# Optimization experiments

Hardware: AMD Instinct MI355X
Metric: run time of the kernel (lower is better)

Reference implementation:

```python
import jax, jax.numpy as jnp
import numpy as np

N_EMBD = 1568  # 2 * 784, hard-coded in the source module
HEAD_SIZE = 128
BATCH = 16384


def setup_inputs() -> dict:
    key = jax.random.key(0)
    kx, kq, kk, kv = jax.random.split(key, 4)
    x = jax.random.normal(kx, (BATCH, N_EMBD), dtype=jnp.float32)
    wq = jax.random.normal(kq, (N_EMBD, HEAD_SIZE), dtype=jnp.float32) * (N_EMBD ** -0.5)
    wk = jax.random.normal(kk, (N_EMBD, HEAD_SIZE), dtype=jnp.float32) * (N_EMBD ** -0.5)
    wv = jax.random.normal(kv, (N_EMBD, HEAD_SIZE), dtype=jnp.float32) * (N_EMBD ** -0.5)
    return {"x": x, "wq": wq, "wk": wk, "wv": wv}


def reference(x, wq, wk, wv):
    # x: [B, N]; projections (bias-free Linear): [B, H]
    B, N = x.shape
    q = x @ wq
    k = x @ wk
    v = x @ wv
    # Outer-product score matrix per batch element: [B, H, H]
    attn = jnp.einsum('bi,bj->bij', q, k) * (N ** -0.5)  # scale uses FEATURE dim N, as in source
    attn = jax.nn.softmax(attn, axis=-1)
    # dropout is identity in eval mode
    out = jnp.einsum('bij,bj->bi', attn, v)  # [B, H]
    return out
```

## Files before the change

kernel.cpp:

```cpp
#include <hip/hip_runtime.h>
#include <stdint.h>

typedef unsigned short u16;
typedef __bf16 bf16x8 __attribute__((ext_vector_type(8)));
typedef float f32x4 __attribute__((ext_vector_type(4)));

#define M_ROWS 16384
#define K_DIM  1568
#define H_DIM  128
#define NQ     384
#define MT     32
#define BK     32
#define NSTEP  49
#define K0LEN  768
#define K1LEN  800
#define ASTR   808
#define PSTR   132
#define KSTRIDE (NQ * BK)
#define SCALE  0.02525381361380526f
#define LOG2E  1.4426950408889634f

__device__ __forceinline__ u16 f32_to_bf16_rne(float f) {
    uint32_t u = __float_as_uint(f);
    uint32_t r = (u + 0x7FFFu + ((u >> 16) & 1u)) >> 16;
    return (u16)r;
}

#define MFMA(a, b, c) __builtin_amdgcn_mfma_f32_16x16x32_bf16(a, b, c, 0, 0, 0)

__global__ __launch_bounds__(256) void wtrans_kernel(
    const float* __restrict__ wq, const float* __restrict__ wk,
    const float* __restrict__ wv, u16* __restrict__ wt2)
{
    __shared__ u16 tile[32][33];
    const float* w = (blockIdx.z == 0) ? wq : (blockIdx.z == 1) ? wk : wv;
    const int k0 = blockIdx.x * 32;
    const int nloc0 = blockIdx.y * 32;
    const int ng0 = blockIdx.z * 128 + nloc0;

    const int tn = threadIdx.x & 31;
    const int tk = threadIdx.x >> 5;
    #pragma unroll
    for (int p = 0; p < 4; p++) {
        int kk = tk + p * 8;
        tile[kk][tn] = f32_to_bf16_rne(w[(size_t)(k0 + kk) * H_DIM + nloc0 + tn]);
    }
    __syncthreads();

    const int klo = threadIdx.x & 31;
    const int tn2 = threadIdx.x >> 5;
    u16* dst = wt2 + (size_t)(k0 >> 5) * KSTRIDE;
    #pragma unroll
    for (int p = 0; p < 4; p++) {
        int nn = tn2 + p * 8;
        dst[(size_t)(ng0 + nn) * 32 + klo] = tile[klo][nn];
    }
}

__global__ __launch_bounds__(512) void fused_kernel(
    const float* __restrict__ x,
    const u16* __restrict__ wt2,
    float* __restrict__ out)
{
    __shared__ char smem[MT * ASTR * 2];
    u16*  Abuf = (u16*)smem;
    float (*Pq)[PSTR] = (float (*)[PSTR])smem;
    float (*Pk)[PSTR] = (float (*)[PSTR])(smem + MT * PSTR * 4);
    float (*Pv)[PSTR] = (float (*)[PSTR])(smem + 2 * MT * PSTR * 4);

    const int tid  = threadIdx.x;
    const int lane = tid & 63;
    const int wave = tid >> 6;
    const int lrow = lane & 15;
    const int quad = lane >> 4;
    const int m0   = blockIdx.x * MT;

    const u16* bp[3];
    #pragma unroll
    for (int nt = 0; nt < 3; nt++) {
        int ng = wave * 48 + nt * 16 + lrow;
        bp[nt] = wt2 + (size_t)ng * 32 + quad * 8;
    }

    const int srow = tid >> 4;
    const int st16 = tid & 15;
    const float* xrow = x + (size_t)(m0 + srow) * K_DIM;

    f32x4 acc[2][3] = {};
    const u16* a_ld0 = &Abuf[(0 * 16 + lrow) * ASTR + quad * 8];
    const u16* a_ld1 = &Abuf[(1 * 16 + lrow) * ASTR + quad * 8];

    for (int i = st16; i < K0LEN / 4; i += 16) {
        f32x4 f = __builtin_nontemporal_load((const f32x4*)(xrow + i * 4));
        union { u16 h[4]; uint2 v; } p;
        p.h[0] = f32_to_bf16_rne(f.x); p.h[1] = f32_to_bf16_rne(f.y);
        p.h[2] = f32_to_bf16_rne(f.z); p.h[3] = f32_to_bf16_rne(f.w);
        *(uint2*)&Abuf[srow * ASTR + i * 4] = p.v;
    }

    bf16x8 B0[3], B1[3];
    #pragma unroll
    for (int nt = 0; nt < 3; nt++) {
        B0[nt] = *(const bf16x8*)(bp[nt]);
        B1[nt] = *(const bf16x8*)(bp[nt] + KSTRIDE);
    }
    __syncthreads();

    #pragma unroll 2
    for (int it = 0; it < 24; it++) {
        const size_t kpf = (size_t)(it + 2) * KSTRIDE;
        bf16x8 B2_0 = *(const bf16x8*)(bp[0] + kpf);
        bf16x8 B2_1 = *(const bf16x8*)(bp[1] + kpf);
        bf16x8 B2_2 = *(const bf16x8*)(bp[2] + kpf);

        bf16x8 a0 = *(const bf16x8*)(a_ld0 + it * BK);
        bf16x8 a1 = *(const bf16x8*)(a_ld1 + it * BK);

        acc[0][0] = MFMA(a0, B0[0], acc[0][0]);
        acc[1][0] = MFMA(a1, B0[0], acc[1][0]);
        acc[0][1] = MFMA(a0, B0[1], acc[0][1]);
        acc[1][1] = MFMA(a1, B0[1], acc[1][1]);
        acc[0][2] = MFMA(a0, B0[2], acc[0][2]);
        acc[1][2] = MFMA(a1, B0[2], acc[1][2]);

        B0[0] = B1[0]; B0[1] = B1[1]; B0[2] = B1[2];
        B1[0] = B2_0;  B1[1] = B2_1;  B1[2] = B2_2;
    }
    __syncthreads();

    for (int i = st16; i < K1LEN / 4; i += 16) {
        f32x4 f = __builtin_nontemporal_load((const f32x4*)(xrow + K0LEN + i * 4));
        union { u16 h[4]; uint2 v; } p;
        p.h[0] = f32_to_bf16_rne(f.x); p.h[1] = f32_to_bf16_rne(f.y);
        p.h[2] = f32_to_bf16_rne(f.z); p.h[3] = f32_to_bf16_rne(f.w);
        *(uint2*)&Abuf[srow * ASTR + i * 4] = p.v;
    }
    __syncthreads();

    #pragma unroll 2
    for (int it = 0; it < 25; it++) {
        int kg = 24 + it + 2;
        if (kg > NSTEP - 1) kg = NSTEP - 1;
        const size_t kpf = (size_t)kg * KSTRIDE;
        bf16x8 B2_0 = *(const bf16x8*)(bp[0] + kpf);
        bf16x8 B2_1 = *(const bf16x8*)(bp[1] + kpf);
        bf16x8 B2_2 = *(const bf16x8*)(bp[2] + kpf);

        bf16x8 a0 = *(const bf16x8*)(a_ld0 + it * BK);
        bf16x8 a1 = *(const bf16x8*)(a_ld1 + it * BK);

        acc[0][0] = MFMA(a0, B0[0], acc[0][0]);
        acc[1][0] = MFMA(a1, B0[0], acc[1][0]);
        acc[0][1] = MFMA(a0, B0[1], acc[0][1]);
        acc[1][1] = MFMA(a1, B0[1], acc[1][1]);
        acc[0][2] = MFMA(a0, B0[2], acc[0][2]);
        acc[1][2] = MFMA(a1, B0[2], acc[1][2]);

        B0[0] = B1[0]; B0[1] = B1[1]; B0[2] = B1[2];
        B1[0] = B2_0;  B1[1] = B2_1;  B1[2] = B2_2;
    }
    __syncthreads();

    #pragma unroll
    for (int mt = 0; mt < 2; mt++) {
        #pragma unroll
        for (int nt = 0; nt < 3; nt++) {
            const int base = wave * 48 + nt * 16;
            const int sel  = base >> 7;
            const int col  = (base & 127) + lrow;
            const int mrow = mt * 16 + quad * 4;
            if (sel == 0) {
                #pragma unroll
                for (int r = 0; r < 4; r++)
                    Pq[mrow + r][col] = acc[mt][nt][r] * (SCALE * LOG2E);
            } else if (sel == 1) {
                #pragma unroll
                for (int r = 0; r < 4; r++)
                    Pk[mrow + r][col] = acc[mt][nt][r];
            } else {
                #pragma unroll
                for (int r = 0; r < 4; r++)
                    Pv[mrow + r][col] = acc[mt][nt][r];
            }
        }
    }
    __syncthreads();

    const int r   = tid >> 4;
    const int sub = tid & 15;

    float qq[8], num[8], den[8];
    #pragma unroll
    for (int ii = 0; ii < 8; ii++) {
        qq[ii]  = Pq[r][sub * 8 + ii];
        num[ii] = 0.f;
        den[ii] = 0.f;
    }

    #pragma unroll 4
    for (int j = 0; j < 128; j++) {
        float kj = Pk[r][j];
        float vj = Pv[r][j];
        #pragma unroll
        for (int ii = 0; ii < 8; ii++) {
            float e = __builtin_amdgcn_exp2f(qq[ii] * kj);
            den[ii] += e;
            num[ii] += e * vj;
        }
    }

    float* op = out + (size_t)(m0 + r) * H_DIM + sub * 8;
    #pragma unroll
    for (int g = 0; g < 2; g++) {
        f32x4 o;
        o.x = num[4 * g + 0] / den[4 * g + 0];
        o.y = num[4 * g + 1] / den[4 * g + 1];
        o.z = num[4 * g + 2] / den[4 * g + 2];
        o.w = num[4 * g + 3] / den[4 * g + 3];
        __builtin_nontemporal_store(o, (f32x4*)(op + 4 * g));
    }
}

extern "C" void kernel_launch(void* const* d_in, const int* in_sizes, int n_in,
                              void* d_out, int out_size, void* d_ws, size_t ws_size,
                              hipStream_t stream)
{
    const float* x  = (const float*)d_in[0];
    const float* wq = (const float*)d_in[1];
    const float* wk = (const float*)d_in[2];
    const float* wv = (const float*)d_in[3];
    float* out = (float*)d_out;

    u16* wt2 = (u16*)d_ws;

    wtrans_kernel<<<dim3(K_DIM / 32, H_DIM / 32, 3), 256, 0, stream>>>(wq, wk, wv, wt2);
    fused_kernel<<<M_ROWS / MT, 512, 0, stream>>>(x, wt2, out);
}
```

Baseline: 212.9 us.

## Double-buffer x chunks in LDS to overlap global loads with MFMA

Replaces the two-phase load-then-compute scheme with four 384-column chunks staged through two LDS buffers. Global loads for the next chunk are issued while MFMAs run on the current one, and a small tail buffer holds the last 32 columns. It also switches to packed bf16 conversion (v_cvt_pk_bf16_f32), packed f32 math in the softmax loop, vectorized LDS reads, and adds an occupancy hint in launch bounds. This hides x-load latency behind compute, at the cost of more registers and some risk of spills.

New measurement: 204.1 us. 4.1% less time.

```diff
diff --git a/kernel.cpp b/kernel.cpp
--- a/kernel.cpp
+++ b/kernel.cpp
@@ -4,6 +4,7 @@
 typedef unsigned short u16;
 typedef __bf16 bf16x8 __attribute__((ext_vector_type(8)));
 typedef float f32x4 __attribute__((ext_vector_type(4)));
+typedef float f32x2 __attribute__((ext_vector_type(2)));
 
 #define M_ROWS 16384
 #define K_DIM  1568
@@ -12,9 +13,10 @@
 #define MT     32
 #define BK     32
 #define NSTEP  49
-#define K0LEN  768
-#define K1LEN  800
-#define ASTR   808
+#define CH_F   384
+#define ASTR   392
+#define TSTR   40
+#define ABUF   (MT * ASTR)
 #define PSTR   132
 #define KSTRIDE (NQ * BK)
 #define SCALE  0.02525381361380526f
@@ -24,6 +26,27 @@
     uint32_t u = __float_as_uint(f);
     uint32_t r = (u + 0x7FFFu + ((u >> 16) & 1u)) >> 16;
     return (u16)r;
+}
+
+__device__ __forceinline__ uint32_t cvt_pk(float lo, float hi) {
+    uint32_t d;
+    asm("v_cvt_pk_bf16_f32 %0, %1, %2" : "=v"(d) : "v"(lo), "v"(hi));
+    return d;
+}
+
+__device__ __forceinline__ f32x2 pk_mul(f32x2 a, f32x2 b) {
+    f32x2 d; asm("v_pk_mul_f32 %0, %1, %2" : "=v"(d) : "v"(a), "v"(b)); return d;
+}
+__device__ __forceinline__ f32x2 pk_add(f32x2 a, f32x2 b) {
+    f32x2 d; asm("v_pk_add_f32 %0, %1, %2" : "=v"(d) : "v"(a), "v"(b)); return d;
+}
+__device__ __forceinline__ f32x2 pk_fma(f32x2 a, f32x2 b, f32x2 c) {
+    f32x2 d; asm("v_pk_fma_f32 %0, %1, %2, %3" : "=v"(d) : "v"(a), "v"(b), "v"(c)); return d;
+}
+
+__device__ __forceinline__ void cvt_wr8(u16* dst, f32x4 v) {
+    uint2 t; t.x = cvt_pk(v.x, v.y); t.y = cvt_pk(v.z, v.w);
+    *(uint2*)dst = t;
 }
 
 #define MFMA(a, b, c) __builtin_amdgcn_mfma_f32_16x16x32_bf16(a, b, c, 0, 0, 0)
@@ -57,13 +80,15 @@
     }
 }
 
-__global__ __launch_bounds__(512) void fused_kernel(
+__global__ __launch_bounds__(512, 4) void fused_kernel(
     const float* __restrict__ x,
     const u16* __restrict__ wt2,
     float* __restrict__ out)
 {
-    __shared__ char smem[MT * ASTR * 2];
-    u16*  Abuf = (u16*)smem;
+    __shared__ char smem[2 * ABUF * 2 + MT * TSTR * 2];
+    u16* A0 = (u16*)smem;
+    u16* A1 = A0 + ABUF;
+    u16* TB = A1 + ABUF;
     float (*Pq)[PSTR] = (float (*)[PSTR])smem;
     float (*Pk)[PSTR] = (float (*)[PSTR])(smem + MT * PSTR * 4);
     float (*Pv)[PSTR] = (float (*)[PSTR])(smem + 2 * MT * PSTR * 4);
@@ -75,150 +100,158 @@
     const int quad = lane >> 4;
     const int m0   = blockIdx.x * MT;
 
-    const u16* bp[3];
-    #pragma unroll
-    for (int nt = 0; nt < 3; nt++) {
-        int ng = wave * 48 + nt * 16 + lrow;
-        bp[nt] = wt2 + (size_t)ng * 32 + quad * 8;
-    }
+    const u16* bp0 = wt2 + (size_t)(wave * 48 +  0 + lrow) * 32 + quad * 8;
+    const u16* bp1 = wt2 + (size_t)(wave * 48 + 16 + lrow) * 32 + quad * 8;
+    const u16* bp2 = wt2 + (size_t)(wave * 48 + 32 + lrow) * 32 + quad * 8;
 
     const int srow = tid >> 4;
     const int st16 = tid & 15;
     const float* xrow = x + (size_t)(m0 + srow) * K_DIM;
-
-    f32x4 acc[2][3] = {};
-    const u16* a_ld0 = &Abuf[(0 * 16 + lrow) * ASTR + quad * 8];
-    const u16* a_ld1 = &Abuf[(1 * 16 + lrow) * ASTR + quad * 8];
-
-    for (int i = st16; i < K0LEN / 4; i += 16) {
-        f32x4 f = __builtin_nontemporal_load((const f32x4*)(xrow + i * 4));
-        union { u16 h[4]; uint2 v; } p;
-        p.h[0] = f32_to_bf16_rne(f.x); p.h[1] = f32_to_bf16_rne(f.y);
-        p.h[2] = f32_to_bf16_rne(f.z); p.h[3] = f32_to_bf16_rne(f.w);
-        *(uint2*)&Abuf[srow * ASTR + i * 4] = p.v;
-    }
-
-    bf16x8 B0[3], B1[3];
-    #pragma unroll
-    for (int nt = 0; nt < 3; nt++) {
-        B0[nt] = *(const bf16x8*)(bp[nt]);
-        B1[nt] = *(const bf16x8*)(bp[nt] + KSTRIDE);
-    }
-    __syncthreads();
-
-    #pragma unroll 2
-    for (int it = 0; it < 24; it++) {
-        const size_t kpf = (size_t)(it + 2) * KSTRIDE;
-        bf16x8 B2_0 = *(const bf16x8*)(bp[0] + kpf);
-        bf16x8 B2_1 = *(const bf16x8*)(bp[1] + kpf);
-        bf16x8 B2_2 = *(const bf16x8*)(bp[2] + kpf);
-
-        bf16x8 a0 = *(const bf16x8*)(a_ld0 + it * BK);
-        bf16x8 a1 = *(const bf16x8*)(a_ld1 + it * BK);
-
-        acc[0][0] = MFMA(a0, B0[0], acc[0][0]);
-        acc[1][0] = MFMA(a1, B0[0], acc[1][0]);
-        acc[0][1] = MFMA(a0, B0[1], acc[0][1]);
-        acc[1][1] = MFMA(a1, B0[1], acc[1][1]);
-        acc[0][2] = MFMA(a0, B0[2], acc[0][2]);
-        acc[1][2] = MFMA(a1, B0[2], acc[1][2]);
-
-        B0[0] = B1[0]; B0[1] = B1[1]; B0[2] = B1[2];
-        B1[0] = B2_0;  B1[1] = B2_1;  B1[2] = B2_2;
-    }
-    __syncthreads();
-
-    for (int i = st16; i < K1LEN / 4; i += 16) {
-        f32x4 f = __builtin_nontemporal_load((const f32x4*)(xrow + K0LEN + i * 4));
-        union { u16 h[4]; uint2 v; } p;
-        p.h[0] = f32_to_bf16_rne(f.x); p.h[1] = f32_to_bf16_rne(f.y);
-        p.h[2] = f32_to_bf16_rne(f.z); p.h[3] = f32_to_bf16_rne(f.w);
-        *(uint2*)&Abuf[srow * ASTR + i * 4] = p.v;
-    }
-    __syncthreads();
-
-    #pragma unroll 2
-    for (int it = 0; it < 25; it++) {
-        int kg = 24 + it + 2;
-        if (kg > NSTEP - 1) kg = NSTEP - 1;
-        const size_t kpf = (size_t)kg * KSTRIDE;
-        bf16x8 B2_0 = *(const bf16x8*)(bp[0] + kpf);
-        bf16x8 B2_1 = *(const bf16x8*)(bp[1] + kpf);
-        bf16x8 B2_2 = *(const bf16x8*)(bp[2] + kpf);
-
-        bf16x8 a0 = *(const bf16x8*)(a_ld0 + it * BK);
-        bf16x8 a1 = *(const bf16x8*)(a_ld1 + it * BK);
-
-        acc[0][0] = MFMA(a0, B0[0], acc[0][0]);
-        acc[1][0] = MFMA(a1, B0[0], acc[1][0]);
-        acc[0][1] = MFMA(a0, B0[1], acc[0][1]);
-        acc[1][1] = MFMA(a1, B0[1], acc[1][1]);
-        acc[0][2] = MFMA(a0, B0[2], acc[0][2]);
-        acc[1][2] = MFMA(a1, B0[2], acc[1][2]);
-
-        B0[0] = B1[0]; B0[1] = B1[1]; B0[2] = B1[2];
-        B1[0] = B2_0;  B1[1] = B2_1;  B1[2] = B2_2;
-    }
-    __syncthreads();
-
-    #pragma unroll
-    for (int mt = 0; mt < 2; mt++) {
-        #pragma unroll
-        for (int nt = 0; nt < 3; nt++) {
-            const int base = wave * 48 + nt * 16;
-            const int sel  = base >> 7;
-            const int col  = (base & 127) + lrow;
-            const int mrow = mt * 16 + quad * 4;
-            if (sel == 0) {
-                #pragma unroll
-                for (int r = 0; r < 4; r++)
-                    Pq[mrow + r][col] = acc[mt][nt][r] * (SCALE * LOG2E);
-            } else if (sel == 1) {
-                #pragma unroll
-                for (int r = 0; r < 4; r++)
-                    Pk[mrow + r][col] = acc[mt][nt][r];
-            } else {
-                #pragma unroll
-                for (int r = 0; r < 4; r++)
-                    Pv[mrow + r][col] = acc[mt][nt][r];
-            }
-        }
-    }
+    u16* wb0 = A0 + srow * ASTR + st16 * 4;
+    u16* wb1 = A1 + srow * ASTR + st16 * 4;
+
+    const u16* aA0 = A0 + lrow * ASTR + quad * 8;
+    const u16* aA1 = A0 + (16 + lrow) * ASTR + quad * 8;
+    const u16* aB0 = A1 + lrow * ASTR + quad * 8;
+    const u16* aB1 = A1 + (16 + lrow) * ASTR + quad * 8;
+
+#define NTLD4(off) __builtin_nontemporal_load((const f32x4*)(xrow + (off)))
+#define LOADC(S, OFF) do { \
+    S##0 = NTLD4((OFF) + st16 * 4 +   0); \
+    S##1 = NTLD4((OFF) + st16 * 4 +  64); \
+    S##2 = NTLD4((OFF) + st16 * 4 + 128); \
+    S##3 = NTLD4((OFF) + st16 * 4 + 192); \
+    S##4 = NTLD4((OFF) + st16 * 4 + 256); \
+    S##5 = NTLD4((OFF) + st16 * 4 + 320); \
+} while (0)
+#define WRITEC(WB, S) do { \
+    cvt_wr8((WB) +   0, S##0); cvt_wr8((WB) +  64, S##1); \
+    cvt_wr8((WB) + 128, S##2); cvt_wr8((WB) + 192, S##3); \
+    cvt_wr8((WB) + 256, S##4); cvt_wr8((WB) + 320, S##5); \
+} while (0)
+
+    f32x4 acc00 = {}, acc01 = {}, acc02 = {};
+    f32x4 acc10 = {}, acc11 = {}, acc12 = {};
+    f32x4 s00, s01, s02, s03, s04, s05;
+    f32x4 s10, s11, s12, s13, s14, s15;
+
+    LOADC(s0, 0);
+    f32x2 tl = __builtin_nontemporal_load((const f32x2*)(xrow + 1536 + st16 * 2));
+    LOADC(s1, CH_F);
+    WRITEC(wb0, s0);
+    *(uint32_t*)(TB + srow * TSTR + st16 * 2) = cvt_pk(tl.x, tl.y);
+
+    bf16x8 Ba0 = *(const bf16x8*)(bp0);
+    bf16x8 Ba1 = *(const bf16x8*)(bp1);
+    bf16x8 Ba2 = *(const bf16x8*)(bp2);
+    bf16x8 Bb0 = *(const bf16x8*)(bp0 + KSTRIDE);
+    bf16x8 Bb1 = *(const bf16x8*)(bp1 + KSTRIDE);
+    bf16x8 Bb2 = *(const bf16x8*)(bp2 + KSTRIDE);
+    __syncthreads();
+
+#define KSTEP(P0, P1, IT, G) do { \
+    int gp = (G) + 2; if (gp > NSTEP - 1) gp = NSTEP - 1; \
+    const size_t o = (size_t)gp * KSTRIDE; \
+    bf16x8 Bc0 = *(const bf16x8*)(bp0 + o); \
+    bf16x8 Bc1 = *(const bf16x8*)(bp1 + o); \
+    bf16x8 Bc2 = *(const bf16x8*)(bp2 + o); \
+    bf16x8 a0 = *(const bf16x8*)((P0) + (IT) * BK); \
+    bf16x8 a1 = *(const bf16x8*)((P1) + (IT) * BK); \
+    acc00 = MFMA(a0, Ba0, acc00); acc10 = MFMA(a1, Ba0, acc10); \
+    acc01 = MFMA(a0, Ba1, acc01); acc11 = MFMA(a1, Ba1, acc11); \
+    acc02 = MFMA(a0, Ba2, acc02); acc12 = MFMA(a1, Ba2, acc12); \
+    Ba0 = Bb0; Ba1 = Bb1; Ba2 = Bb2; Bb0 = Bc0; Bb1 = Bc1; Bb2 = Bc2; \
+} while (0)
+
+    WRITEC(wb1, s1);
+    LOADC(s0, 2 * CH_F);
+    #pragma unroll
+    for (int it = 0; it < 12; ++it) KSTEP(aA0, aA1, it, it);
+    __syncthreads();
+
+    WRITEC(wb0, s0);
+    LOADC(s1, 3 * CH_F);
+    #pragma unroll
+    for (int it = 0; it < 12; ++it) KSTEP(aB0, aB1, it, 12 + it);
+    __syncthreads();
+
+    WRITEC(wb1, s1);
+    #pragma unroll
+    for (int it = 0; it < 12; ++it) KSTEP(aA0, aA1, it, 24 + it);
+    __syncthreads();
+
+    #pragma unroll
+    for (int it = 0; it < 12; ++it) KSTEP(aB0, aB1, it, 36 + it);
+
+    {
+        bf16x8 a0 = *(const bf16x8*)(TB + lrow * TSTR + quad * 8);
+        bf16x8 a1 = *(const bf16x8*)(TB + (16 + lrow) * TSTR + quad * 8);
+        acc00 = MFMA(a0, Ba0, acc00); acc10 = MFMA(a1, Ba0, acc10);
+        acc01 = MFMA(a0, Ba1, acc01); acc11 = MFMA(a1, Ba1, acc11);
+        acc02 = MFMA(a0, Ba2, acc02); acc12 = MFMA(a1, Ba2, acc12);
+    }
+    __syncthreads();
+
+#define SCAT(ACC, MTi, NTi) do { \
+    const int base = wave * 48 + (NTi) * 16; \
+    const int sel  = base >> 7; \
+    const int col  = (base & 127) + lrow; \
+    const int mrow = (MTi) * 16 + quad * 4; \
+    if (sel == 0)      { _Pragma("unroll") for (int rr = 0; rr < 4; rr++) Pq[mrow + rr][col] = ACC[rr] * (SCALE * LOG2E); } \
+    else if (sel == 1) { _Pragma("unroll") for (int rr = 0; rr < 4; rr++) Pk[mrow + rr][col] = ACC[rr]; } \
+    else               { _Pragma("unroll") for (int rr = 0; rr < 4; rr++) Pv[mrow + rr][col] = ACC[rr]; } \
+} while (0)
+
+    SCAT(acc00, 0, 0); SCAT(acc01, 0, 1); SCAT(acc02, 0, 2);
+    SCAT(acc10, 1, 0); SCAT(acc11, 1, 1); SCAT(acc12, 1, 2);
     __syncthreads();
 
     const int r   = tid >> 4;
     const int sub = tid & 15;
 
-    float qq[8], num[8], den[8];
-    #pragma unroll
-    for (int ii = 0; ii < 8; ii++) {
-        qq[ii]  = Pq[r][sub * 8 + ii];
-        num[ii] = 0.f;
-        den[ii] = 0.f;
-    }
-
-    #pragma unroll 4
-    for (int j = 0; j < 128; j++) {
-        float kj = Pk[r][j];
-        float vj = Pv[r][j];
+    f32x4 qa = *(const f32x4*)&Pq[r][sub * 8];
+    f32x4 qb = *(const f32x4*)&Pq[r][sub * 8 + 4];
+    f32x2 q01; q01.x = qa.x; q01.y = qa.y;
+    f32x2 q23; q23.x = qa.z; q23.y = qa.w;
+    f32x2 q45; q45.x = qb.x; q45.y = qb.y;
+    f32x2 q67; q67.x = qb.z; q67.y = qb.w;
+
+    f32x2 d01 = {}, d23 = {}, d45 = {}, d67 = {};
+    f32x2 n01 = {}, n23 = {}, n45 = {}, n67 = {};
+
+    #pragma unroll 2
+    for (int j4 = 0; j4 < 32; ++j4) {
+        f32x4 k4 = *(const f32x4*)&Pk[r][j4 * 4];
+        f32x4 v4 = *(const f32x4*)&Pv[r][j4 * 4];
         #pragma unroll
-        for (int ii = 0; ii < 8; ii++) {
-            float e = __builtin_amdgcn_exp2f(qq[ii] * kj);
-            den[ii] += e;
-            num[ii] += e * vj;
+        for (int jj = 0; jj < 4; ++jj) {
+            float kj = k4[jj];
+            float vj = v4[jj];
+            f32x2 kk; kk.x = kj; kk.y = kj;
+            f32x2 vv; vv.x = vj; vv.y = vj;
+            f32x2 sc01 = pk_mul(q01, kk);
+            f32x2 sc23 = pk_mul(q23, kk);
+            f32x2 sc45 = pk_mul(q45, kk);
+            f32x2 sc67 = pk_mul(q67, kk);
+            f32x2 e01; e01.x = __builtin_amdgcn_exp2f(sc01.x); e01.y = __builtin_amdgcn_exp2f(sc01.y);
+            f32x2 e23; e23.x = __builtin_amdgcn_exp2f(sc23.x); e23.y = __builtin_amdgcn_exp2f(sc23.y);
+            f32x2 e45; e45.x = __builtin_amdgcn_exp2f(sc45.x); e45.y = __builtin_amdgcn_exp2f(sc45.y);
+            f32x2 e67; e67.x = __builtin_amdgcn_exp2f(sc67.x); e67.y = __builtin_amdgcn_exp2f(sc67.y);
+            d01 = pk_add(d01, e01); n01 = pk_fma(e01, vv, n01);
+            d23 = pk_add(d23, e23); n23 = pk_fma(e23, vv, n23);
+            d45 = pk_add(d45, e45); n45 = pk_fma(e45, vv, n45);
+            d67 = pk_add(d67, e67); n67 = pk_fma(e67, vv, n67);
         }
     }
 
     float* op = out + (size_t)(m0 + r) * H_DIM + sub * 8;
-    #pragma unroll
-    for (int g = 0; g < 2; g++) {
-        f32x4 o;
-        o.x = num[4 * g + 0] / den[4 * g + 0];
-        o.y = num[4 * g + 1] / den[4 * g + 1];
-        o.z = num[4 * g + 2] / den[4 * g + 2];
-        o.w = num[4 * g + 3] / den[4 * g + 3];
-        __builtin_nontemporal_store(o, (f32x4*)(op + 4 * g));
-    }
+    f32x4 o0, o1;
+    o0.x = n01.x / d01.x; o0.y = n01.y / d01.y;
+    o0.z = n23.x / d23.x; o0.w = n23.y / d23.y;
+    o1.x = n45.x / d45.x; o1.y = n45.y / d45.y;
+    o1.z = n67.x / d67.x; o1.w = n67.y / d67.y;
+    __builtin_nontemporal_store(o0, (f32x4*)(op));
+    __builtin_nontemporal_store(o1, (f32x4*)(op + 4));
 }
 
 extern "C" void kernel_launch(void* const* d_in, const int* in_sizes, int n_in,
```
